# Optimization experiments

Measured on AMD Instinct MI355X. Metric: run time of the kernel, lower is better.

## Reference

```python
import jax, jax.numpy as jnp
import numpy as np

N, G, E, H, OUT, MAX_N = 131072, 256, 384, 6, 256, 1024
DH = E // H  # 64


def _make_sizes():
    # variable-length segments summing exactly to N, each in [1, MAX_N]
    rng = np.random.default_rng(0)
    raw = rng.integers(128, 896, G).astype(np.int64)
    diff = int(N - raw.sum())
    q, r = divmod(diff, G)
    sizes = raw + q
    sizes[:r] += 1
    assert sizes.sum() == N and sizes.min() >= 1 and sizes.max() <= MAX_N
    return sizes


def setup_inputs() -> dict:
    key = jax.random.key(0)
    ks = jax.random.split(key, 8)
    s = 1.0 / np.sqrt(E)
    return {
        "node_feat": jax.random.normal(ks[0], (N, E), jnp.float32),
        "sizes": jnp.asarray(_make_sizes(), jnp.int32),
        "query": jax.random.normal(ks[1], (E,), jnp.float32),
        "Wq": jax.random.normal(ks[2], (E, E), jnp.float32) * s,
        "bq": jnp.zeros((E,), jnp.float32),
        "Wk": jax.random.normal(ks[3], (E, E), jnp.float32) * s,
        "bk": jnp.zeros((E,), jnp.float32),
        "Wv": jax.random.normal(ks[4], (E, E), jnp.float32) * s,
        "bv": jnp.zeros((E,), jnp.float32),
        "Wo": jax.random.normal(ks[5], (E, E), jnp.float32) * s,
        "bo": jnp.zeros((E,), jnp.float32),
        "Wp": jax.random.normal(ks[6], (OUT, E), jnp.float32) * s,
        "bp": jnp.zeros((OUT,), jnp.float32),
    }


def reference(node_feat, sizes, query, Wq, bq, Wk, bk, Wv, bv, Wo, bo, Wp, bp):
    # segment offsets and padded gather indices
    offsets = jnp.cumsum(sizes) - sizes                      # [G]
    pos = jnp.arange(MAX_N)
    idx = jnp.clip(offsets[:, None] + pos[None, :], 0, N - 1)  # [G, MAX_N]
    mask = pos[None, :] < sizes[:, None]                     # [G, MAX_N]

    # project K/V on the flat node table (one big GEMM), then gather into padded form
    k_flat = node_feat @ Wk.T + bk                           # [N, E]
    v_flat = node_feat @ Wv.T + bv
    k = k_flat[idx].reshape(G, MAX_N, H, DH)
    v = v_flat[idx].reshape(G, MAX_N, H, DH)

    # single shared query token, pre-scaled (PyTorch MHA scales q by 1/sqrt(head_dim))
    q = ((query @ Wq.T + bq) * (1.0 / np.sqrt(DH))).reshape(H, DH)

    scores = jnp.einsum('hd,gnhd->ghn', q, k)                # [G, H, MAX_N]
    scores = jnp.where(mask[:, None, :], scores, -1e30)
    attn = jax.nn.softmax(scores, axis=-1)
    pooled = jnp.einsum('ghn,gnhd->ghd', attn, v).reshape(G, E)

    out = pooled @ Wo.T + bo                                 # MHA out_proj
    return out @ Wp.T + bp                                   # final proj  [G, OUT]
```

## Files before the change

kernel.cpp:

```cpp
#include <hip/hip_runtime.h>
#include <math.h>

#define NN 131072
#define G  256
#define E  384
#define H  6
#define DH 64
#define OUTD 256
#define MAXN 1024

#define WS_QK   0
#define WS_C    2304
#define WS_OFF  2432
#define WS_QV   2944
#define WS_SC   4096
#define WS_XBAR (4096 + NN*6)
#define WS_WVT  (WS_XBAR + G*H*E)
#define WS_WOT  (WS_WVT + E*E)
#define WS_WPT  (WS_WOT + E*E)

__global__ __launch_bounds__(256) void k0a_scan_qv(
    const int* __restrict__ sizes, const float* __restrict__ query,
    const float* __restrict__ Wq, const float* __restrict__ bq,
    float* __restrict__ wsf) {
  __shared__ int s_scan[G];
  const int tid = threadIdx.x;
  if (blockIdx.x == 0) {
    s_scan[tid] = sizes[tid];
    __syncthreads();
    for (int d = 1; d < G; d <<= 1) {
      int t = (tid >= d) ? s_scan[tid - d] : 0;
      __syncthreads();
      s_scan[tid] += t;
      __syncthreads();
    }
    int* offs = (int*)(wsf + WS_OFF);
    offs[tid] = s_scan[tid] - sizes[tid];
  } else {
    const int lane = tid & 63;
    const int i = (blockIdx.x - 1) * 4 + (tid >> 6);
    float a = 0.f;
#pragma unroll
    for (int j = 0; j < 6; j++)
      a += Wq[(size_t)i * E + j * 64 + lane] * query[j * 64 + lane];
#pragma unroll
    for (int mm = 1; mm < 64; mm <<= 1) a += __shfl_xor(a, mm, 64);
    if (lane == 0) wsf[WS_QV + i] = 0.125f * (a + bq[i]);
  }
}

__global__ __launch_bounds__(256) void k0b_qk(
    const float* __restrict__ Wk, const float* __restrict__ bk,
    float* __restrict__ wsf) {
  __shared__ float qv_s[64];
  __shared__ float ps[256];
  const int h = blockIdx.x / 6, ec = blockIdx.x % 6;
  const int tid = threadIdx.x;
  if (tid < 64) qv_s[tid] = wsf[WS_QV + h * 64 + tid];
  __syncthreads();
  const int el = tid & 63, dq = tid >> 6;
  float a = 0.f;
#pragma unroll 4
  for (int d = dq * 16; d < dq * 16 + 16; d++)
    a += qv_s[d] * Wk[(size_t)(h * 64 + d) * E + ec * 64 + el];
  ps[tid] = a;
  __syncthreads();
  if (tid < 64)
    wsf[WS_QK + h * E + ec * 64 + tid] =
        ps[tid] + ps[64 + tid] + ps[128 + tid] + ps[192 + tid];
  if (ec == 0 && tid < 64) {
    float p = qv_s[tid] * bk[h * 64 + tid];
#pragma unroll
    for (int mm = 1; mm < 64; mm <<= 1) p += __shfl_xor(p, mm, 64);
    if (tid == 0) wsf[WS_C + h] = p;
  }
}

__global__ __launch_bounds__(256) void k0t_transpose(
    const float* __restrict__ Wv, const float* __restrict__ Wo,
    const float* __restrict__ Wp, float* __restrict__ wsf) {
  __shared__ float s[64][65];
  const int b = blockIdx.x;
  const float* src;
  float* dst;
  int R, tr, tc;
  if (b < 36)      { src = Wv; dst = wsf + WS_WVT; R = 384; tr = b / 6;        tc = b % 6; }
  else if (b < 72) { src = Wo; dst = wsf + WS_WOT; R = 384; tr = (b - 36) / 6; tc = (b - 36) % 6; }
  else             { src = Wp; dst = wsf + WS_WPT; R = 256; tr = (b - 72) / 6; tc = (b - 72) % 6; }
  const int r0 = tr * 64, c0 = tc * 64;
#pragma unroll
  for (int k = 0; k < 16; k++) {
    int idx = k * 256 + threadIdx.x;
    int r = idx >> 6, cc = idx & 63;
    s[r][cc] = src[(size_t)(r0 + r) * E + c0 + cc];
  }
  __syncthreads();
#pragma unroll
  for (int k = 0; k < 16; k++) {
    int idx = k * 256 + threadIdx.x;
    int cc = idx >> 6, r = idx & 63;
    dst[(size_t)(c0 + cc) * R + r0 + r] = s[r][cc];
  }
}

__global__ __launch_bounds__(256) void k1_scores(
    const float* __restrict__ x, const float* __restrict__ wsf,
    float* __restrict__ scores) {
  __shared__ float qk_l[8 * 292];
  __shared__ float c_s[8];
  const int tid = threadIdx.x;
  for (int idx = tid; idx < 2304; idx += 256) {
    int sub = idx / 288, rem = idx % 288;
    int h = rem / 48, r2 = rem % 48, j = r2 >> 2, r = r2 & 3;
    qk_l[sub * 292 + h * 48 + j * 4 + r] =
        wsf[WS_QK + h * E + (j * 8 + sub) * 4 + r];
  }
  if (tid < 8) c_s[tid] = (tid < 6) ? wsf[WS_C + tid] : 0.f;
  __syncthreads();

  const int lane = tid & 63;
  const int sub = lane & 7, nod = lane >> 3;
  const int wid = blockIdx.x * 4 + (tid >> 6);
  const int n0 = wid * 32;
  const float4* x4 = (const float4*)x;

  float acc[4][6];
#pragma unroll
  for (int o = 0; o < 4; o++)
#pragma unroll
    for (int h = 0; h < 6; h++) acc[o][h] = 0.f;

#pragma unroll 4
  for (int j = 0; j < 12; j++) {
    float4 qk4[6];
#pragma unroll
    for (int h = 0; h < 6; h++)
      qk4[h] = *(const float4*)&qk_l[sub * 292 + h * 48 + j * 4];
    float4 xv[4];
#pragma unroll
    for (int o = 0; o < 4; o++)
      xv[o] = x4[(size_t)(n0 + o * 8 + nod) * 96 + j * 8 + sub];
#pragma unroll
    for (int o = 0; o < 4; o++)
#pragma unroll
      for (int h = 0; h < 6; h++)
        acc[o][h] += qk4[h].x * xv[o].x + qk4[h].y * xv[o].y
                   + qk4[h].z * xv[o].z + qk4[h].w * xv[o].w;
  }
#pragma unroll
  for (int o = 0; o < 4; o++) {
#pragma unroll
    for (int h = 0; h < 6; h++) {
      acc[o][h] += __shfl_xor(acc[o][h], 1, 64);
      acc[o][h] += __shfl_xor(acc[o][h], 2, 64);
      acc[o][h] += __shfl_xor(acc[o][h], 4, 64);
    }
    float v = acc[o][0];
#pragma unroll
    for (int h = 1; h < 6; h++) v = (sub == h) ? acc[o][h] : v;
    if (sub < 6)
      scores[(size_t)(n0 + o * 8 + nod) * H + sub] = v + c_s[sub];
  }
}

#define K2T 512
__global__ __launch_bounds__(K2T) void k2_pool(
    const float* __restrict__ x, const int* __restrict__ sizes,
    const float* __restrict__ wsf, float* __restrict__ xbar) {
  __shared__ float pbuf[H][MAXN];
  __shared__ float redm[8][H];
  __shared__ float redl[8][H];
  __shared__ float psum[4][H][128];
  const int tid = threadIdx.x;
  const int w = tid >> 6;
  const int c = blockIdx.x % 3;
  const int g = blockIdx.x / 3;
  const int* offs = (const int*)(wsf + WS_OFF);
  const int off = offs[g];
  const int Ng = sizes[g];
  const float* sc = wsf + WS_SC + (size_t)off * H;

  float m[H];
#pragma unroll
  for (int h = 0; h < H; h++) m[h] = -3.0e38f;
  for (int n = tid; n < Ng; n += K2T) {
#pragma unroll
    for (int h = 0; h < H; h++) {
      float s = sc[(size_t)n * H + h];
      pbuf[h][n] = s;
      m[h] = fmaxf(m[h], s);
    }
  }
#pragma unroll
  for (int h = 0; h < H; h++)
#pragma unroll
    for (int mm = 1; mm < 64; mm <<= 1) m[h] = fmaxf(m[h], __shfl_xor(m[h], mm, 64));
  if ((tid & 63) == 0)
#pragma unroll
    for (int h = 0; h < H; h++) redm[w][h] = m[h];
  __syncthreads();
#pragma unroll
  for (int h = 0; h < H; h++) {
    m[h] = redm[0][h];
#pragma unroll
    for (int ww = 1; ww < 8; ww++) m[h] = fmaxf(m[h], redm[ww][h]);
  }

  float l[H];
#pragma unroll
  for (int h = 0; h < H; h++) l[h] = 0.f;
  for (int n = tid; n < Ng; n += K2T) {
#pragma unroll
    for (int h = 0; h < H; h++) {
      float p = __expf(pbuf[h][n] - m[h]);
      pbuf[h][n] = p;
      l[h] += p;
    }
  }
  const int NgP = (Ng + 31) & ~31;
  for (int n = Ng + tid; n < NgP; n += K2T)
#pragma unroll
    for (int h = 0; h < H; h++) pbuf[h][n] = 0.f;
#pragma unroll
  for (int h = 0; h < H; h++)
#pragma unroll
    for (int mm = 1; mm < 64; mm <<= 1) l[h] += __shfl_xor(l[h], mm, 64);
  if ((tid & 63) == 0)
#pragma unroll
    for (int h = 0; h < H; h++) redl[w][h] = l[h];
  __syncthreads();
  float inv[H];
#pragma unroll
  for (int h = 0; h < H; h++) {
    float s = redl[0][h];
#pragma unroll
    for (int ww = 1; ww < 8; ww++) s += redl[ww][h];
    inv[h] = 1.f / s;
  }

  const int col = tid & 127;
  const int np = tid >> 7;
  const int q4 = NgP >> 2;
  const int n0 = np * q4, n1 = n0 + q4;
  float acc[H];
#pragma unroll
  for (int h = 0; h < H; h++) acc[h] = 0.f;
  const float* xcol = x + (size_t)off * E + c * 128 + col;
  for (int n = n0; n < n1; n += 8) {
    float xv[8];
#pragma unroll
    for (int k = 0; k < 8; k++) {
      int nn = n + k;
      nn = nn < Ng ? nn : Ng - 1;
      xv[k] = xcol[(size_t)nn * E];
    }
#pragma unroll
    for (int h = 0; h < H; h++) {
      const float4 p0 = *(const float4*)&pbuf[h][n];
      const float4 p1 = *(const float4*)&pbuf[h][n + 4];
      acc[h] += p0.x * xv[0] + p0.y * xv[1] + p0.z * xv[2] + p0.w * xv[3]
              + p1.x * xv[4] + p1.y * xv[5] + p1.z * xv[6] + p1.w * xv[7];
    }
  }
#pragma unroll
  for (int h = 0; h < H; h++) psum[np][h][col] = acc[h];
  __syncthreads();
  if (np == 0) {
#pragma unroll
    for (int h = 0; h < H; h++) {
      float a = psum[0][h][col] + psum[1][h][col] + psum[2][h][col] + psum[3][h][col];
      xbar[((size_t)g * H + h) * E + c * 128 + col] = a * inv[h];
    }
  }
}

__global__ __launch_bounds__(768) void k3_group(
    const float* __restrict__ xbar, const float* __restrict__ wvt,
    const float* __restrict__ wot, const float* __restrict__ wpt,
    const float* __restrict__ bv, const float* __restrict__ bo,
    const float* __restrict__ bp, float* __restrict__ out) {
  __shared__ float xb[H * E];
  __shared__ float pooled[E];
  __shared__ float om[E];
  __shared__ float ps[768];
  const int tid = threadIdx.x;
  const int g = blockIdx.x;

  for (int i = tid; i < H * E; i += 768) xb[i] = xbar[(size_t)g * (H * E) + i];
  __syncthreads();

  {
    const int i = tid % 384, ks = tid / 384;
    const float* xh = xb + (i >> 6) * E + ks * 192;
    const float* wp_ = wvt + (size_t)(ks * 192) * E + i;
    float a0 = 0.f, a1 = 0.f, a2 = 0.f, a3 = 0.f;
#pragma unroll 4
    for (int e = 0; e < 192; e += 4) {
      a0 += wp_[(size_t)(e + 0) * E] * xh[e + 0];
      a1 += wp_[(size_t)(e + 1) * E] * xh[e + 1];
      a2 += wp_[(size_t)(e + 2) * E] * xh[e + 2];
      a3 += wp_[(size_t)(e + 3) * E] * xh[e + 3];
    }
    ps[tid] = (a0 + a1) + (a2 + a3);
  }
  __syncthreads();
  if (tid < 384) pooled[tid] = ps[tid] + ps[384 + tid] + bv[tid];
  __syncthreads();

  {
    const int i = tid % 384, ks = tid / 384;
    const float* xh = pooled + ks * 192;
    const float* wp_ = wot + (size_t)(ks * 192) * E + i;
    float a0 = 0.f, a1 = 0.f, a2 = 0.f, a3 = 0.f;
#pragma unroll 4
    for (int e = 0; e < 192; e += 4) {
      a0 += wp_[(size_t)(e + 0) * E] * xh[e + 0];
      a1 += wp_[(size_t)(e + 1) * E] * xh[e + 1];
      a2 += wp_[(size_t)(e + 2) * E] * xh[e + 2];
      a3 += wp_[(size_t)(e + 3) * E] * xh[e + 3];
    }
    ps[tid] = (a0 + a1) + (a2 + a3);
  }
  __syncthreads();
  if (tid < 384) om[tid] = ps[tid] + ps[384 + tid] + bo[tid];
  __syncthreads();

  {
    const int o = tid % 256, ks = tid / 256;
    const float* xh = om + ks * 128;
    const float* wp_ = wpt + (size_t)(ks * 128) * OUTD + o;
    float a0 = 0.f, a1 = 0.f, a2 = 0.f, a3 = 0.f;
#pragma unroll 4
    for (int e = 0; e < 128; e += 4) {
      a0 += wp_[(size_t)(e + 0) * OUTD] * xh[e + 0];
      a1 += wp_[(size_t)(e + 1) * OUTD] * xh[e + 1];
      a2 += wp_[(size_t)(e + 2) * OUTD] * xh[e + 2];
      a3 += wp_[(size_t)(e + 3) * OUTD] * xh[e + 3];
    }
    ps[tid] = (a0 + a1) + (a2 + a3);
  }
  __syncthreads();
  if (tid < 256)
    out[(size_t)g * OUTD + tid] = ps[tid] + ps[256 + tid] + ps[512 + tid] + bp[tid];
}

extern "C" void kernel_launch(void* const* d_in, const int* in_sizes, int n_in,
                              void* d_out, int out_size, void* d_ws, size_t ws_size,
                              hipStream_t stream) {
  const float* x     = (const float*)d_in[0];
  const int*   sizes = (const int*)d_in[1];
  const float* query = (const float*)d_in[2];
  const float* Wq    = (const float*)d_in[3];
  const float* bq    = (const float*)d_in[4];
  const float* Wk    = (const float*)d_in[5];
  const float* bk    = (const float*)d_in[6];
  const float* Wv    = (const float*)d_in[7];
  const float* bv    = (const float*)d_in[8];
  const float* Wo    = (const float*)d_in[9];
  const float* bo    = (const float*)d_in[10];
  const float* Wp    = (const float*)d_in[11];
  const float* bp    = (const float*)d_in[12];
  float* wsf = (float*)d_ws;
  float* out = (float*)d_out;

  hipLaunchKernelGGL(k0a_scan_qv, dim3(97), dim3(256), 0, stream,
                     sizes, query, Wq, bq, wsf);
  hipLaunchKernelGGL(k0b_qk, dim3(36), dim3(256), 0, stream, Wk, bk, wsf);
  hipLaunchKernelGGL(k0t_transpose, dim3(96), dim3(256), 0, stream,
                     Wv, Wo, Wp, wsf);
  hipLaunchKernelGGL(k1_scores, dim3(1024), dim3(256), 0, stream,
                     x, wsf, wsf + WS_SC);
  hipLaunchKernelGGL(k2_pool, dim3(768), dim3(K2T), 0, stream,
                     x, sizes, wsf, wsf + WS_XBAR);
  hipLaunchKernelGGL(k3_group, dim3(G), dim3(768), 0, stream,
                     wsf + WS_XBAR, wsf + WS_WVT, wsf + WS_WOT, wsf + WS_WPT,
                     bv, bo, bp, out);
}
```

Before: 384.9 us.

## Fuse score and pooling kernels into chunked split-softmax with cross-chunk merge

```diff
diff --git a/kernel.cpp b/kernel.cpp
--- a/kernel.cpp
+++ b/kernel.cpp
@@ -9,13 +9,16 @@
 #define OUTD 256
 #define MAXN 1024
 
+#define CHK 256
+#define SLOTS 4
+#define PART_STRIDE 2316
+
 #define WS_QK   0
 #define WS_C    2304
 #define WS_OFF  2432
 #define WS_QV   2944
-#define WS_SC   4096
-#define WS_XBAR (4096 + NN*6)
-#define WS_WVT  (WS_XBAR + G*H*E)
+#define WS_PART 4096
+#define WS_WVT  (WS_PART + G*SLOTS*PART_STRIDE)
 #define WS_WOT  (WS_WVT + E*E)
 #define WS_WPT  (WS_WOT + E*E)
 
@@ -103,190 +106,172 @@
   }
 }
 
-__global__ __launch_bounds__(256) void k1_scores(
-    const float* __restrict__ x, const float* __restrict__ wsf,
-    float* __restrict__ scores) {
+#define PB 264
+__global__ __launch_bounds__(512) void k12_fused(
+    const float* __restrict__ x, const int* __restrict__ sizes,
+    float* __restrict__ wsf) {
   __shared__ float qk_l[8 * 292];
   __shared__ float c_s[8];
+  __shared__ float pbuf[H * PB];
+  __shared__ float psum[4][H][128];
+  const int g = blockIdx.x & 255, s = blockIdx.x >> 8;
+  const int Ng = sizes[g];
+  const int rem = Ng - s * CHK;
+  if (rem <= 0) return;
+  const int clen = rem < CHK ? rem : CHK;
+  const int n0 = ((const int*)(wsf + WS_OFF))[g] + s * CHK;
   const int tid = threadIdx.x;
-  for (int idx = tid; idx < 2304; idx += 256) {
-    int sub = idx / 288, rem = idx % 288;
-    int h = rem / 48, r2 = rem % 48, j = r2 >> 2, r = r2 & 3;
+
+  for (int idx = tid; idx < 2304; idx += 512) {
+    int sub = idx / 288, r3 = idx % 288;
+    int h = r3 / 48, r2 = r3 % 48, j = r2 >> 2, r = r2 & 3;
     qk_l[sub * 292 + h * 48 + j * 4 + r] =
         wsf[WS_QK + h * E + (j * 8 + sub) * 4 + r];
   }
   if (tid < 8) c_s[tid] = (tid < 6) ? wsf[WS_C + tid] : 0.f;
   __syncthreads();
 
-  const int lane = tid & 63;
+  const int lane = tid & 63, w = tid >> 6;
   const int sub = lane & 7, nod = lane >> 3;
-  const int wid = blockIdx.x * 4 + (tid >> 6);
-  const int n0 = wid * 32;
   const float4* x4 = (const float4*)x;
-
-  float acc[4][6];
-#pragma unroll
-  for (int o = 0; o < 4; o++)
-#pragma unroll
-    for (int h = 0; h < 6; h++) acc[o][h] = 0.f;
-
-#pragma unroll 4
-  for (int j = 0; j < 12; j++) {
-    float4 qk4[6];
-#pragma unroll
-    for (int h = 0; h < 6; h++)
-      qk4[h] = *(const float4*)&qk_l[sub * 292 + h * 48 + j * 4];
-    float4 xv[4];
+  {
+    const int base = w * 32;
+    float acc[4][6];
 #pragma unroll
     for (int o = 0; o < 4; o++)
-      xv[o] = x4[(size_t)(n0 + o * 8 + nod) * 96 + j * 8 + sub];
-#pragma unroll
-    for (int o = 0; o < 4; o++)
+#pragma unroll
+      for (int h = 0; h < 6; h++) acc[o][h] = 0.f;
+#pragma unroll 4
+    for (int j = 0; j < 12; j++) {
+      float4 qk4[6];
 #pragma unroll
       for (int h = 0; h < 6; h++)
-        acc[o][h] += qk4[h].x * xv[o].x + qk4[h].y * xv[o].y
-                   + qk4[h].z * xv[o].z + qk4[h].w * xv[o].w;
-  }
-#pragma unroll
-  for (int o = 0; o < 4; o++) {
-#pragma unroll
-    for (int h = 0; h < 6; h++) {
-      acc[o][h] += __shfl_xor(acc[o][h], 1, 64);
-      acc[o][h] += __shfl_xor(acc[o][h], 2, 64);
-      acc[o][h] += __shfl_xor(acc[o][h], 4, 64);
-    }
-    float v = acc[o][0];
-#pragma unroll
-    for (int h = 1; h < 6; h++) v = (sub == h) ? acc[o][h] : v;
-    if (sub < 6)
-      scores[(size_t)(n0 + o * 8 + nod) * H + sub] = v + c_s[sub];
-  }
-}
-
-#define K2T 512
-__global__ __launch_bounds__(K2T) void k2_pool(
-    const float* __restrict__ x, const int* __restrict__ sizes,
-    const float* __restrict__ wsf, float* __restrict__ xbar) {
-  __shared__ float pbuf[H][MAXN];
-  __shared__ float redm[8][H];
-  __shared__ float redl[8][H];
-  __shared__ float psum[4][H][128];
-  const int tid = threadIdx.x;
-  const int w = tid >> 6;
-  const int c = blockIdx.x % 3;
-  const int g = blockIdx.x / 3;
-  const int* offs = (const int*)(wsf + WS_OFF);
-  const int off = offs[g];
-  const int Ng = sizes[g];
-  const float* sc = wsf + WS_SC + (size_t)off * H;
-
-  float m[H];
-#pragma unroll
-  for (int h = 0; h < H; h++) m[h] = -3.0e38f;
-  for (int n = tid; n < Ng; n += K2T) {
-#pragma unroll
-    for (int h = 0; h < H; h++) {
-      float s = sc[(size_t)n * H + h];
-      pbuf[h][n] = s;
-      m[h] = fmaxf(m[h], s);
-    }
-  }
-#pragma unroll
-  for (int h = 0; h < H; h++)
-#pragma unroll
-    for (int mm = 1; mm < 64; mm <<= 1) m[h] = fmaxf(m[h], __shfl_xor(m[h], mm, 64));
-  if ((tid & 63) == 0)
-#pragma unroll
-    for (int h = 0; h < H; h++) redm[w][h] = m[h];
-  __syncthreads();
-#pragma unroll
-  for (int h = 0; h < H; h++) {
-    m[h] = redm[0][h];
-#pragma unroll
-    for (int ww = 1; ww < 8; ww++) m[h] = fmaxf(m[h], redm[ww][h]);
-  }
-
-  float l[H];
-#pragma unroll
-  for (int h = 0; h < H; h++) l[h] = 0.f;
-  for (int n = tid; n < Ng; n += K2T) {
-#pragma unroll
-    for (int h = 0; h < H; h++) {
-      float p = __expf(pbuf[h][n] - m[h]);
-      pbuf[h][n] = p;
-      l[h] += p;
-    }
-  }
-  const int NgP = (Ng + 31) & ~31;
-  for (int n = Ng + tid; n < NgP; n += K2T)
-#pragma unroll
-    for (int h = 0; h < H; h++) pbuf[h][n] = 0.f;
-#pragma unroll
-  for (int h = 0; h < H; h++)
-#pragma unroll
-    for (int mm = 1; mm < 64; mm <<= 1) l[h] += __shfl_xor(l[h], mm, 64);
-  if ((tid & 63) == 0)
-#pragma unroll
-    for (int h = 0; h < H; h++) redl[w][h] = l[h];
-  __syncthreads();
-  float inv[H];
-#pragma unroll
-  for (int h = 0; h < H; h++) {
-    float s = redl[0][h];
-#pragma unroll
-    for (int ww = 1; ww < 8; ww++) s += redl[ww][h];
-    inv[h] = 1.f / s;
-  }
-
-  const int col = tid & 127;
-  const int np = tid >> 7;
-  const int q4 = NgP >> 2;
-  const int n0 = np * q4, n1 = n0 + q4;
-  float acc[H];
-#pragma unroll
-  for (int h = 0; h < H; h++) acc[h] = 0.f;
-  const float* xcol = x + (size_t)off * E + c * 128 + col;
-  for (int n = n0; n < n1; n += 8) {
-    float xv[8];
-#pragma unroll
-    for (int k = 0; k < 8; k++) {
-      int nn = n + k;
-      nn = nn < Ng ? nn : Ng - 1;
-      xv[k] = xcol[(size_t)nn * E];
-    }
-#pragma unroll
-    for (int h = 0; h < H; h++) {
-      const float4 p0 = *(const float4*)&pbuf[h][n];
-      const float4 p1 = *(const float4*)&pbuf[h][n + 4];
-      acc[h] += p0.x * xv[0] + p0.y * xv[1] + p0.z * xv[2] + p0.w * xv[3]
-              + p1.x * xv[4] + p1.y * xv[5] + p1.z * xv[6] + p1.w * xv[7];
-    }
-  }
-#pragma unroll
-  for (int h = 0; h < H; h++) psum[np][h][col] = acc[h];
-  __syncthreads();
-  if (np == 0) {
-#pragma unroll
-    for (int h = 0; h < H; h++) {
-      float a = psum[0][h][col] + psum[1][h][col] + psum[2][h][col] + psum[3][h][col];
-      xbar[((size_t)g * H + h) * E + c * 128 + col] = a * inv[h];
-    }
+        qk4[h] = *(const float4*)&qk_l[sub * 292 + h * 48 + j * 4];
+      float4 xv[4];
+#pragma unroll
+      for (int o = 0; o < 4; o++) {
+        int nn = base + o * 8 + nod;
+        nn = nn < clen ? nn : clen - 1;
+        xv[o] = x4[(size_t)(n0 + nn) * 96 + j * 8 + sub];
+      }
+#pragma unroll
+      for (int o = 0; o < 4; o++)
+#pragma unroll
+        for (int h = 0; h < 6; h++)
+          acc[o][h] += qk4[h].x * xv[o].x + qk4[h].y * xv[o].y
+                     + qk4[h].z * xv[o].z + qk4[h].w * xv[o].w;
+    }
+#pragma unroll
+    for (int o = 0; o < 4; o++) {
+#pragma unroll
+      for (int h = 0; h < 6; h++) {
+        acc[o][h] += __shfl_xor(acc[o][h], 1, 64);
+        acc[o][h] += __shfl_xor(acc[o][h], 2, 64);
+        acc[o][h] += __shfl_xor(acc[o][h], 4, 64);
+      }
+      float v = acc[o][0];
+#pragma unroll
+      for (int h = 1; h < 6; h++) v = (sub == h) ? acc[o][h] : v;
+      if (sub < 6) {
+        int nn = base + o * 8 + nod;
+        pbuf[sub * PB + nn] = (nn < clen) ? v + c_s[sub] : -1.0e30f;
+      }
+    }
+  }
+  __syncthreads();
+
+  float* pslot = wsf + WS_PART + (size_t)(g * SLOTS + s) * PART_STRIDE;
+  if (w < 6) {
+    float vals[4];
+#pragma unroll
+    for (int k = 0; k < 4; k++) vals[k] = pbuf[w * PB + lane + k * 64];
+    float m = fmaxf(fmaxf(vals[0], vals[1]), fmaxf(vals[2], vals[3]));
+#pragma unroll
+    for (int mm = 1; mm < 64; mm <<= 1) m = fmaxf(m, __shfl_xor(m, mm, 64));
+    float lsum = 0.f;
+#pragma unroll
+    for (int k = 0; k < 4; k++) {
+      float e = __expf(vals[k] - m);
+      pbuf[w * PB + lane + k * 64] = e;
+      lsum += e;
+    }
+#pragma unroll
+    for (int mm = 1; mm < 64; mm <<= 1) lsum += __shfl_xor(lsum, mm, 64);
+    if (lane == 0) { pslot[2304 + w] = m; pslot[2310 + w] = lsum; }
+  }
+  __syncthreads();
+
+  const int col = tid & 127, np = tid >> 7;
+  for (int c = 0; c < 3; c++) {
+    float acc[6];
+#pragma unroll
+    for (int h = 0; h < 6; h++) acc[h] = 0.f;
+    const float* xcol = x + (size_t)n0 * E + c * 128 + col;
+    for (int n = np * 64; n < np * 64 + 64; n += 8) {
+      float xv[8];
+#pragma unroll
+      for (int k = 0; k < 8; k++) {
+        int nn = n + k;
+        nn = nn < clen ? nn : clen - 1;
+        xv[k] = xcol[(size_t)nn * E];
+      }
+#pragma unroll
+      for (int h = 0; h < 6; h++) {
+        const float4 p0 = *(const float4*)&pbuf[h * PB + n];
+        const float4 p1 = *(const float4*)&pbuf[h * PB + n + 4];
+        acc[h] += p0.x * xv[0] + p0.y * xv[1] + p0.z * xv[2] + p0.w * xv[3]
+                + p1.x * xv[4] + p1.y * xv[5] + p1.z * xv[6] + p1.w * xv[7];
+      }
+    }
+#pragma unroll
+    for (int h = 0; h < 6; h++) psum[np][h][col] = acc[h];
+    __syncthreads();
+    if (np == 0)
+#pragma unroll
+      for (int h = 0; h < 6; h++)
+        pslot[h * E + c * 128 + col] =
+            psum[0][h][col] + psum[1][h][col] + psum[2][h][col] + psum[3][h][col];
+    __syncthreads();
   }
 }
 
 __global__ __launch_bounds__(768) void k3_group(
-    const float* __restrict__ xbar, const float* __restrict__ wvt,
-    const float* __restrict__ wot, const float* __restrict__ wpt,
+    const float* __restrict__ wsf, const int* __restrict__ sizes,
     const float* __restrict__ bv, const float* __restrict__ bo,
     const float* __restrict__ bp, float* __restrict__ out) {
   __shared__ float xb[H * E];
   __shared__ float pooled[E];
   __shared__ float om[E];
   __shared__ float ps[768];
+  __shared__ float wgt[SLOTS][H];
+  __shared__ float linv[H];
   const int tid = threadIdx.x;
   const int g = blockIdx.x;
-
-  for (int i = tid; i < H * E; i += 768) xb[i] = xbar[(size_t)g * (H * E) + i];
+  const int nch = (sizes[g] + CHK - 1) / CHK;
+  const float* pg = wsf + WS_PART + (size_t)g * SLOTS * PART_STRIDE;
+  const float* wvt = wsf + WS_WVT;
+  const float* wot = wsf + WS_WOT;
+  const float* wpt = wsf + WS_WPT;
+
+  if (tid < H) {
+    float m = -3.0e38f;
+    for (int s = 0; s < nch; s++)
+      m = fmaxf(m, pg[(size_t)s * PART_STRIDE + 2304 + tid]);
+    float L = 0.f;
+    for (int s = 0; s < nch; s++) {
+      float wv_ = __expf(pg[(size_t)s * PART_STRIDE + 2304 + tid] - m);
+      wgt[s][tid] = wv_;
+      L += pg[(size_t)s * PART_STRIDE + 2310 + tid] * wv_;
+    }
+    linv[tid] = 1.f / L;
+  }
+  __syncthreads();
+  for (int idx = tid; idx < H * E; idx += 768) {
+    int h = idx / E;
+    float a = 0.f;
+    for (int s = 0; s < nch; s++) a += pg[(size_t)s * PART_STRIDE + idx] * wgt[s][h];
+    xb[idx] = a * linv[h];
+  }
   __syncthreads();
 
   {
@@ -368,11 +353,8 @@
   hipLaunchKernelGGL(k0b_qk, dim3(36), dim3(256), 0, stream, Wk, bk, wsf);
   hipLaunchKernelGGL(k0t_transpose, dim3(96), dim3(256), 0, stream,
                      Wv, Wo, Wp, wsf);
-  hipLaunchKernelGGL(k1_scores, dim3(1024), dim3(256), 0, stream,
-                     x, wsf, wsf + WS_SC);
-  hipLaunchKernelGGL(k2_pool, dim3(768), dim3(K2T), 0, stream,
-                     x, sizes, wsf, wsf + WS_XBAR);
+  hipLaunchKernelGGL(k12_fused, dim3(G * SLOTS), dim3(512), 0, stream,
+                     x, sizes, wsf);
   hipLaunchKernelGGL(k3_group, dim3(G), dim3(768), 0, stream,
-                     wsf + WS_XBAR, wsf + WS_WVT, wsf + WS_WOT, wsf + WS_WPT,
-                     bv, bo, bp, out);
-}
+                     wsf, sizes, bv, bo, bp, out);
+}
```

Measured after the change: 373.2 us. -3.0%, faster.
